# Kernel tuning notes

Hardware: AMD Instinct MI355X
Metric: run time of the kernel (lower is better)

Reference implementation:

```python
import jax, jax.numpy as jnp
import numpy as np

I1, H1, H2, NC = 38, 50, 15, 14

def _lstm(x, w_ih, w_hh, b_ih, b_hh):
    # x: [B, T, I]; weights in torch layout: w_ih [4H, I], w_hh [4H, H]
    # torch gate order: i, f, g, o
    B, T, _ = x.shape
    H = w_hh.shape[1]
    gx = jnp.einsum('bti,gi->btg', x, w_ih) + b_ih + b_hh  # [B, T, 4H]
    gx = jnp.swapaxes(gx, 0, 1)  # [T, B, 4H]

    def step(carry, g_t):
        h, c = carry
        g = g_t + h @ w_hh.T
        i_g, f_g, c_g, o_g = jnp.split(g, 4, axis=-1)
        i_g = jax.nn.sigmoid(i_g)
        f_g = jax.nn.sigmoid(f_g)
        o_g = jax.nn.sigmoid(o_g)
        c = f_g * c + i_g * jnp.tanh(c_g)
        h = o_g * jnp.tanh(c)
        return (h, c), h

    init = (jnp.zeros((B, H), x.dtype), jnp.zeros((B, H), x.dtype))
    _, hs = jax.lax.scan(step, init, gx)  # hs: [T, B, H]
    return jnp.swapaxes(hs, 0, 1)  # [B, T, H]

def setup_inputs() -> dict:
    key = jax.random.key(0)
    ks = jax.random.split(key, 12)
    s1 = 1.0 / np.sqrt(H1)
    s2 = 1.0 / np.sqrt(H2)
    u = lambda k, shape, s: jax.random.uniform(k, shape, jnp.float32, -s, s)
    return {
        'x': jax.random.normal(ks[0], (4096, 256, I1), jnp.float32),
        'w_ih1': u(ks[1], (4 * H1, I1), s1),
        'w_hh1': u(ks[2], (4 * H1, H1), s1),
        'b_ih1': u(ks[3], (4 * H1,), s1),
        'b_hh1': u(ks[4], (4 * H1,), s1),
        'w_ih2': u(ks[5], (4 * H2, H1), s2),
        'w_hh2': u(ks[6], (4 * H2, H2), s2),
        'b_ih2': u(ks[7], (4 * H2,), s2),
        'b_hh2': u(ks[8], (4 * H2,), s2),
        'w_fc': u(ks[9], (NC, H2), s2),
        'b_fc': u(ks[10], (NC,), s2),
    }

def reference(x, w_ih1, w_hh1, b_ih1, b_hh1, w_ih2, w_hh2, b_ih2, b_hh2, w_fc, b_fc):
    out = _lstm(x, w_ih1, w_hh1, b_ih1, b_hh1)          # [B, T, 50]
    # dropout(0.2) is identity in eval mode
    out = _lstm(out, w_ih2, w_hh2, b_ih2, b_hh2)        # [B, T, 15]
    return out[:, -1, :] @ w_fc.T + b_fc                # [B, 14]
```

## Files before the change

### kernel.cpp

```cpp
#include <hip/hip_runtime.h>


typedef _Float16 f16x8 __attribute__((ext_vector_type(8)));
typedef _Float16 f16x2 __attribute__((ext_vector_type(2)));
typedef float    f32x4 __attribute__((ext_vector_type(4)));

#if __has_builtin(__builtin_amdgcn_exp2f)
#define DEV_EXP2(x) __builtin_amdgcn_exp2f(x)
#else
#define DEV_EXP2(x) exp2f(x)
#endif
#if __has_builtin(__builtin_amdgcn_rcpf)
#define DEV_RCP(x) __builtin_amdgcn_rcpf(x)
#else
#define DEV_RCP(x) (1.0f/(x))
#endif

#define I1 38
#define H1 50
#define H2 15
#define NC 14
#define TT 256
#define SB 16
#define XS 136
#define NTH 512
#define L2E 2.885390081777927f
#define L1E 1.442695040888963f

#define MF(A,B,C) __builtin_amdgcn_mfma_f32_16x16x32_f16((A),(B),(C),0,0,0)
#define BARRIER() asm volatile("s_waitcnt lgkmcnt(0)\n\ts_barrier" ::: "memory")

__device__ __forceinline__ float sigm(float v)  { return DEV_RCP(1.f + DEV_EXP2(-L1E * v)); }
__device__ __forceinline__ float tanh_f(float v){ return 1.f - 2.f * DEV_RCP(1.f + DEV_EXP2(L2E * v)); }

__launch_bounds__(NTH, 1)
__global__ void lstm2_fused(const float* __restrict__ x,
                            const float* __restrict__ w_ih1, const float* __restrict__ w_hh1,
                            const float* __restrict__ b_ih1, const float* __restrict__ b_hh1,
                            const float* __restrict__ w_ih2, const float* __restrict__ w_hh2,
                            const float* __restrict__ b_ih2, const float* __restrict__ b_hh2,
                            const float* __restrict__ w_fc, const float* __restrict__ b_fc,
                            float* __restrict__ out)
{
  __shared__ __align__(16) _Float16 bufA[2][SB][XS];

  const int tid  = threadIdx.x;
  const int wv   = tid >> 6;
  const int lane = tid & 63;
  const int lm   = lane & 15;
  const int lk   = lane >> 4;
  const int blk  = blockIdx.x;
  const float* xblk = x + (size_t)blk * SB * TT * I1;

  for (int i = tid; i < 2*SB*XS; i += NTH) ((_Float16*)bufA)[i] = (_Float16)0.f;

  auto welem = [&](bool il1, bool valid, int u, int g, int k) -> _Float16 {
    float w = 0.f;
    if (valid) {
      if (il1) {
        if (k < I1)                w = w_ih1[(g*H1 + u)*I1 + k];
        else if (k < I1 + H1)      w = w_hh1[(g*H1 + u)*H1 + (k - I1)];
      } else {
        if (k >= I1 && k < I1+H1)             w = w_ih2[(g*H2 + u)*H1 + (k - I1)];
        else if (k >= I1+H1 && k < I1+H1+H2)  w = w_hh2[(g*H2 + u)*H2 + (k - I1 - H1)];
      }
    }
    return (_Float16)w;
  };

  const int t1 = wv + 8;
  const int r0 = wv*16 + lm, u0f = r0 >> 2, g0 = r0 & 3;
  const int r1 = t1*16 + lm, q1 = r1 >> 2, g1 = r1 & 3;
  const bool il1f = (q1 < H1);
  const int  u1f = il1f ? q1 : (q1 - H1);
  const bool w16 = (wv == 0);
  const bool c16 = w16 && (lm < 4);

  const bool s1k0 = (wv <= 4);
  const bool s1k3 = (wv >= 4);
  const bool needA3 = w16 || s1k3;

  f16x8 W0[3], W1[4], W16[3];
  #pragma unroll
  for (int ks = 0; ks < 3; ++ks) {
    f16x8 v;
    #pragma unroll
    for (int e = 0; e < 8; ++e) v[e] = welem(true, true, u0f, g0, ks*32 + lk*8 + e);
    W0[ks] = v;
  }
  #pragma unroll
  for (int ks = 0; ks < 4; ++ks) {
    f16x8 v;
    #pragma unroll
    for (int e = 0; e < 8; ++e) v[e] = welem(il1f, true, u1f, g1, ks*32 + lk*8 + e);
    W1[ks] = v;
  }
  #pragma unroll
  for (int j = 0; j < 3; ++j) {
    f16x8 v;
    #pragma unroll
    for (int e = 0; e < 8; ++e) v[e] = welem(false, c16, 14, lm & 3, (j+1)*32 + lk*8 + e);
    W16[j] = v;
  }

  const int uS0 = 4*wv + lk;
  const int d0  = 38 + uS0;
  const int uS1 = 32 + 4*wv + lk;
  const bool il1u = (uS1 < H1);
  const int  uS1r = il1u ? uS1 : (uS1 - H1);
  const int  d1   = il1u ? (38 + uS1) : (88 + uS1r);
  const bool hasC = w16 && (lk == 0);

  float sb0[4], sb1[4], sbC[4];
  #pragma unroll
  for (int m = 0; m < 4; ++m) {
    sb0[m] = b_ih1[m*H1 + uS0] + b_hh1[m*H1 + uS0];
    sb1[m] = il1u ? (b_ih1[m*H1 + uS1] + b_hh1[m*H1 + uS1])
                  : (b_ih2[m*H2 + uS1r] + b_hh2[m*H2 + uS1r]);
    sbC[m] = b_ih2[m*H2 + 14] + b_hh2[m*H2 + 14];
  }

  const bool vx = (tid < SB*19);
  const int s0 = vx ? (tid / 19) : 0, q0 = vx ? (tid % 19) : 0;
  const int gb0 = s0*TT*I1 + 2*q0;
  const int lb0 = s0*XS + 2*q0;

  auto st2 = [&](_Float16* dst, float2 v) {
    f16x2 h; h[0] = (_Float16)v.x; h[1] = (_Float16)v.y;
    *(f16x2*)dst = h;
  };

  __syncthreads();
  if (vx) st2(&bufA[0][0][0] + lb0, *(const float2*)(xblk + gb0));
  float2 xA0 = {0.f, 0.f}, xB0 = {0.f, 0.f};
  if (vx) xA0 = *(const float2*)(xblk + gb0 + I1);
  __syncthreads();

  float cS0 = 0.f, cS1 = 0.f, cC = 0.f;

#define STEP(T, XC0, XN0) do {                                                  \
    _Float16* cur = &bufA[(T) & 1][0][0];                                       \
    _Float16* nxt = &bufA[((T) & 1) ^ 1][0][0];                                 \
    if (vx && (T) + 2 < TT)                                                     \
      XN0 = *(const float2*)(xblk + gb0 + ((T) + 2) * I1);                      \
    f16x8 a0 = *(const f16x8*)(cur + lm*XS +      lk*8);                        \
    f16x8 a1 = *(const f16x8*)(cur + lm*XS + 32 + lk*8);                        \
    f16x8 a2 = *(const f16x8*)(cur + lm*XS + 64 + lk*8);                        \
    f16x8 a3 = (f16x8)(_Float16)0.f;                                            \
    if (needA3) a3 = *(const f16x8*)(cur + lm*XS + 96 + lk*8);                  \
    {                                                                           \
      f32x4 acc = (f32x4){sb0[0], sb0[1], sb0[2], sb0[3]};                      \
      acc = MF(W0[0], a0, acc);                                                 \
      acc = MF(W0[1], a1, acc);                                                 \
      acc = MF(W0[2], a2, acc);                                                 \
      if ((T) < TT) {                                                           \
        float ig = sigm(acc[0]), fg = sigm(acc[1]);                             \
        float gg = tanh_f(acc[2]), og = sigm(acc[3]);                           \
        cS0 = fg*cS0 + ig*gg;                                                   \
        nxt[lm*XS + d0] = (_Float16)(og * tanh_f(cS0));                         \
      }                                                                         \
    }                                                                           \
    {                                                                           \
      f32x4 acc = (f32x4){sb1[0], sb1[1], sb1[2], sb1[3]};                      \
      if (s1k0) acc = MF(W1[0], a0, acc);                                       \
      acc = MF(W1[1], a1, acc);                                                 \
      acc = MF(W1[2], a2, acc);                                                 \
      if (s1k3) acc = MF(W1[3], a3, acc);                                       \
      const bool up = il1u ? ((T) < TT) : ((T) >= 1);                           \
      if (up) {                                                                 \
        float ig = sigm(acc[0]), fg = sigm(acc[1]);                             \
        float gg = tanh_f(acc[2]), og = sigm(acc[3]);                           \
        cS1 = fg*cS1 + ig*gg;                                                   \
        nxt[lm*XS + d1] = (_Float16)(og * tanh_f(cS1));                         \
      }                                                                         \
    }                                                                           \
    if (w16) {                                                                  \
      f32x4 acc = (f32x4){sbC[0], sbC[1], sbC[2], sbC[3]};                      \
      acc = MF(W16[0], a1, acc);                                                \
      acc = MF(W16[1], a2, acc);                                                \
      acc = MF(W16[2], a3, acc);                                                \
      if (hasC && (T) >= 1) {                                                   \
        float ig = sigm(acc[0]), fg = sigm(acc[1]);                             \
        float gg = tanh_f(acc[2]), og = sigm(acc[3]);                           \
        cC = fg*cC + ig*gg;                                                     \
        nxt[lm*XS + 102] = (_Float16)(og * tanh_f(cC));                         \
      }                                                                         \
    }                                                                           \
    if (vx && (T) + 1 < TT) st2(nxt + lb0, XC0);                                \
    BARRIER();                                                                  \
  } while (0)

  int t = 0;
  for (;;) {
    STEP(t, xA0, xB0);
    if (++t > TT) break;
    STEP(t, xB0, xA0);
    if (++t > TT) break;
  }
#undef STEP

  if (tid < SB*NC) {
    int s = tid / NC, n = tid % NC;
    float acc = b_fc[n];
    #pragma unroll
    for (int u = 0; u < H2; ++u)
      acc += (float)bufA[1][s][88 + u] * w_fc[n*H2 + u];
    out[((size_t)blk*SB + s)*NC + n] = acc;
  }
}

extern "C" void kernel_launch(void* const* d_in, const int* in_sizes, int n_in,
                              void* d_out, int out_size, void* d_ws, size_t ws_size,
                              hipStream_t stream) {
  (void)n_in; (void)d_ws; (void)ws_size; (void)out_size;
  const float* x     = (const float*)d_in[0];
  const float* w_ih1 = (const float*)d_in[1];
  const float* w_hh1 = (const float*)d_in[2];
  const float* b_ih1 = (const float*)d_in[3];
  const float* b_hh1 = (const float*)d_in[4];
  const float* w_ih2 = (const float*)d_in[5];
  const float* w_hh2 = (const float*)d_in[6];
  const float* b_ih2 = (const float*)d_in[7];
  const float* b_hh2 = (const float*)d_in[8];
  const float* w_fc  = (const float*)d_in[9];
  const float* b_fc  = (const float*)d_in[10];
  float* out = (float*)d_out;

  const int B = in_sizes[0] / (TT * I1);
  dim3 grid(B / SB), block(NTH);
  lstm2_fused<<<grid, block, 0, stream>>>(x, w_ih1, w_hh1, b_ih1, b_hh1,
                                          w_ih2, w_hh2, b_ih2, b_hh2,
                                          w_fc, b_fc, out);
}
```

Baseline: 167.1 us.

## Precompute next step's input-projection MFMA off the recurrent critical path

Adds a separate double-buffered LDS buffer for x, staged one step further ahead, so the input-projection MFMA (K-chunk 0) for step T+1 is computed at the end of step T. This takes the x-dependent MFMA and its LDS read off the serial h-dependency chain at the start of each step. It also swaps the custom lgkmcnt-wait plus s_barrier for __syncthreads. The cost is extra LDS stores and accumulator registers per step, and __syncthreads may emit heavier waits than the hand-written barrier.

```diff
diff --git a/kernel.cpp b/kernel.cpp
--- a/kernel.cpp
+++ b/kernel.cpp
@@ -23,12 +23,12 @@
 #define TT 256
 #define SB 16
 #define XS 136
+#define XSX 40
 #define NTH 512
 #define L2E 2.885390081777927f
 #define L1E 1.442695040888963f
 
 #define MF(A,B,C) __builtin_amdgcn_mfma_f32_16x16x32_f16((A),(B),(C),0,0,0)
-#define BARRIER() asm volatile("s_waitcnt lgkmcnt(0)\n\ts_barrier" ::: "memory")
 
 __device__ __forceinline__ float sigm(float v)  { return DEV_RCP(1.f + DEV_EXP2(-L1E * v)); }
 __device__ __forceinline__ float tanh_f(float v){ return 1.f - 2.f * DEV_RCP(1.f + DEV_EXP2(L2E * v)); }
@@ -43,6 +43,7 @@
                             float* __restrict__ out)
 {
   __shared__ __align__(16) _Float16 bufA[2][SB][XS];
+  __shared__ __align__(16) _Float16 bufX[2][SB][XSX];
 
   const int tid  = threadIdx.x;
   const int wv   = tid >> 6;
@@ -52,7 +53,8 @@
   const int blk  = blockIdx.x;
   const float* xblk = x + (size_t)blk * SB * TT * I1;
 
-  for (int i = tid; i < 2*SB*XS; i += NTH) ((_Float16*)bufA)[i] = (_Float16)0.f;
+  for (int i = tid; i < 2*SB*XS; i += NTH)  ((_Float16*)bufA)[i] = (_Float16)0.f;
+  for (int i = tid; i < 2*SB*XSX; i += NTH) ((_Float16*)bufX)[i] = (_Float16)0.f;
 
   auto welem = [&](bool il1, bool valid, int u, int g, int k) -> _Float16 {
     float w = 0.f;
@@ -123,7 +125,8 @@
   const bool vx = (tid < SB*19);
   const int s0 = vx ? (tid / 19) : 0, q0 = vx ? (tid % 19) : 0;
   const int gb0 = s0*TT*I1 + 2*q0;
-  const int lb0 = s0*XS + 2*q0;
+  const int lbA = s0*XS + 2*q0;
+  const int lbX = s0*XSX + 2*q0;
 
   auto st2 = [&](_Float16* dst, float2 v) {
     f16x2 h; h[0] = (_Float16)v.x; h[1] = (_Float16)v.y;
@@ -131,10 +134,22 @@
   };
 
   __syncthreads();
-  if (vx) st2(&bufA[0][0][0] + lb0, *(const float2*)(xblk + gb0));
-  float2 xA0 = {0.f, 0.f}, xB0 = {0.f, 0.f};
-  if (vx) xA0 = *(const float2*)(xblk + gb0 + I1);
+  float2 xC = {0.f, 0.f}, xN = {0.f, 0.f};
+  if (vx) {
+    st2(&bufA[0][0][0] + lbA, *(const float2*)(xblk + gb0));
+    xC = *(const float2*)(xblk + gb0 + I1);
+    st2(&bufX[1][0][0] + lbX, xC);
+  }
   __syncthreads();
+
+  f32x4 accX0, accX1;
+  {
+    f16x8 ax = *(const f16x8*)(&bufA[0][0][0] + lm*XS + lk*8);
+    accX0 = (f32x4){sb0[0], sb0[1], sb0[2], sb0[3]};
+    accX0 = MF(W0[0], ax, accX0);
+    accX1 = (f32x4){sb1[0], sb1[1], sb1[2], sb1[3]};
+    if (s1k0) accX1 = MF(W1[0], ax, accX1);
+  }
 
   float cS0 = 0.f, cS1 = 0.f, cC = 0.f;
 
@@ -143,14 +158,12 @@
     _Float16* nxt = &bufA[((T) & 1) ^ 1][0][0];                                 \
     if (vx && (T) + 2 < TT)                                                     \
       XN0 = *(const float2*)(xblk + gb0 + ((T) + 2) * I1);                      \
-    f16x8 a0 = *(const f16x8*)(cur + lm*XS +      lk*8);                        \
     f16x8 a1 = *(const f16x8*)(cur + lm*XS + 32 + lk*8);                        \
     f16x8 a2 = *(const f16x8*)(cur + lm*XS + 64 + lk*8);                        \
     f16x8 a3 = (f16x8)(_Float16)0.f;                                            \
     if (needA3) a3 = *(const f16x8*)(cur + lm*XS + 96 + lk*8);                  \
     {                                                                           \
-      f32x4 acc = (f32x4){sb0[0], sb0[1], sb0[2], sb0[3]};                      \
-      acc = MF(W0[0], a0, acc);                                                 \
+      f32x4 acc = accX0;                                                        \
       acc = MF(W0[1], a1, acc);                                                 \
       acc = MF(W0[2], a2, acc);                                                 \
       if ((T) < TT) {                                                           \
@@ -161,8 +174,7 @@
       }                                                                         \
     }                                                                           \
     {                                                                           \
-      f32x4 acc = (f32x4){sb1[0], sb1[1], sb1[2], sb1[3]};                      \
-      if (s1k0) acc = MF(W1[0], a0, acc);                                       \
+      f32x4 acc = accX1;                                                        \
       acc = MF(W1[1], a1, acc);                                                 \
       acc = MF(W1[2], a2, acc);                                                 \
       if (s1k3) acc = MF(W1[3], a3, acc);                                       \
@@ -186,15 +198,27 @@
         nxt[lm*XS + 102] = (_Float16)(og * tanh_f(cC));                         \
       }                                                                         \
     }                                                                           \
-    if (vx && (T) + 1 < TT) st2(nxt + lb0, XC0);                                \
-    BARRIER();                                                                  \
+      \
+    if ((T) + 1 < TT) {                                                         \
+      f16x8 ax = *(const f16x8*)(&bufX[((T)+1) & 1][0][0] + lm*XSX + lk*8);     \
+      accX0 = (f32x4){sb0[0], sb0[1], sb0[2], sb0[3]};                          \
+      accX0 = MF(W0[0], ax, accX0);                                             \
+      accX1 = (f32x4){sb1[0], sb1[1], sb1[2], sb1[3]};                          \
+      if (s1k0) accX1 = MF(W1[0], ax, accX1);                                   \
+    } else {                                                                    \
+      accX0 = (f32x4){sb0[0], sb0[1], sb0[2], sb0[3]};                          \
+      accX1 = (f32x4){sb1[0], sb1[1], sb1[2], sb1[3]};                          \
+    }                                                                           \
+    if (vx && (T) + 1 < TT) st2(nxt + lbA, XC0);              \
+    if (vx && (T) + 2 < TT) st2(&bufX[(T) & 1][0][0] + lbX, XN0);   \
+    __syncthreads();                                                            \
   } while (0)
 
   int t = 0;
   for (;;) {
-    STEP(t, xA0, xB0);
+    STEP(t, xC, xN);
     if (++t > TT) break;
-    STEP(t, xB0, xA0);
+    STEP(t, xN, xC);
     if (++t > TT) break;
   }
 #undef STEP
```

Result: slower. 185.3 us (+10.9%).
